# Optimization experiments

Hardware: AMD Instinct MI355X
Metric: run time of the kernel (lower is better)

The kernel has to match this reference:

```python
import jax, jax.numpy as jnp
import numpy as np

BETA = 0.25  # commitment loss weight (standard VQ-VAE beta)


def setup_inputs() -> dict:
    key = jax.random.key(0)
    k1, k2 = jax.random.split(key)
    N, D, Q, K = 131072, 128, 4, 1024
    x = jax.random.normal(k1, (N, D), dtype=jnp.float32)
    codebooks = jax.random.normal(k2, (Q, K, D), dtype=jnp.float32)
    return {"x": x, "codebooks": codebooks}


def reference(x, codebooks):
    """Residual VQ: sequentially quantize the residual against each codebook.

    x:         [N, D] float
    codebooks: [Q, K, D] float (one [K, D] codebook per quantizer stage)
    Returns (x_q [N, D], mean_loss scalar, indices [N, Q] int32).
    """
    sg = jax.lax.stop_gradient

    def stage(carry, E):
        residual, x_q = carry                      # [N, D], [N, D]
        # squared euclidean distances: ||r||^2 - 2 r.E^T + ||E||^2  -> [N, K]
        d = (jnp.sum(residual * residual, axis=1, keepdims=True)
             - 2.0 * (residual @ E.T)
             + jnp.sum(E * E, axis=1))
        idx = jnp.argmin(d, axis=1)                # [N]
        q = E[idx]                                 # [N, D] gather
        # codebook loss + beta * commitment loss
        loss = (jnp.mean((q - sg(residual)) ** 2)
                + BETA * jnp.mean((sg(q) - residual) ** 2))
        # straight-through estimator
        q_st = residual + sg(q - residual)
        return (residual - q_st, x_q + q_st), (loss, idx)

    (_, x_q), (losses, idxs) = jax.lax.scan(
        stage, (x, jnp.zeros_like(x)), codebooks)
    mean_loss = jnp.mean(losses)
    all_indices = jnp.transpose(idxs)              # [Q, N] -> [N, Q], stacked dim=-1
    return x_q, mean_loss, all_indices
```

## Files before the change

kernel.cpp:

```cpp
#include <hip/hip_runtime.h>

#define N_ROWS 131072
#define DIM    128
#define QST    4
#define KC     1024
#define BM     128
#define NTH    256
#define PNTH   256
#define NWAVE  4
#define NCHUNK 64
#define EPS    6e-3f
#define FLAGB  (1 << 16)

typedef _Float16 h8  __attribute__((ext_vector_type(8)));
typedef float    fx4 __attribute__((ext_vector_type(4)));

typedef __attribute__((address_space(3))) void lds_void;
typedef const __attribute__((address_space(1))) void glb_void;

#define MFMA16(a, b, c) __builtin_amdgcn_mfma_f32_16x16x32_f16((a), (b), (c), 0, 0, 0)

__global__ void k_prep(const float* __restrict__ cb,
                       double* __restrict__ cvec64, float* __restrict__ cvec32,
                       _Float16* __restrict__ packB) {
  int gid = blockIdx.x * blockDim.x + threadIdx.x;
  if (gid >= QST * KC) return;
  int q = gid >> 10, code = gid & (KC - 1);
  int ch = code >> 4, n = code & 15;
  const float* e = cb + ((size_t)q * KC + code) * DIM;
  double s = 0.0;
  for (int d = 0; d < DIM; d++) {
    float v = e[d];
    s = fma((double)v, (double)v, s);
    int kt = d >> 5, g = (d >> 3) & 3, j = d & 7;
    int lane = g * 16 + n;
    size_t base = ((size_t)q * NCHUNK + ch) * 4096 + (size_t)kt * 1024 + lane * 8 + j;
    _Float16 hh = (_Float16)v;
    packB[base]       = hh;
    packB[base + 512] = (_Float16)(v - (float)hh);
  }
  cvec64[q * KC + code] = s;
  cvec32[q * KC + code] = (float)s;
}

__global__ __launch_bounds__(NTH, 4) void k_stage(
    int st, const float* rin, float* rout, const float* __restrict__ x,
    const float* __restrict__ cb,
    const double* __restrict__ cvec64, const float* __restrict__ cvec32,
    const _Float16* __restrict__ packB,
    float* __restrict__ oidx, float* __restrict__ lpart, int final_stage)
{
  extern __shared__ float smem[];
  _Float16* Bl      = (_Float16*)smem;
  float*    cvecL   = smem + 6144;
  int*      idxs    = (int*)(smem + 7168);
  double*   redd    = (double*)(smem + 7296);
  int*      redi    = (int*)(smem + 7304);
  float*    redf    = smem + 7308;
  int*      flags   = (int*)(smem + 7312);

  const int tid = threadIdx.x;
  const int lane = tid & 63, wv = tid >> 6;
  const int tx = tid & 15;
  const size_t rowbase = (size_t)blockIdx.x * BM;

  const double*   cq64 = cvec64 + st * KC;
  const float*    cq32 = cvec32 + st * KC;
  const float*    Eq   = cb + (size_t)st * KC * DIM;
  const _Float16* PBq  = packB + (size_t)st * 262144;

  for (int i = tid; i < KC; i += NTH) cvecL[i] = cq32[i];

  h8 ah[2][4], al[2][4];
  #pragma unroll
  for (int rt = 0; rt < 2; rt++) {
    const float* rowp = rin + (rowbase + wv * 32 + rt * 16 + (lane & 15)) * (size_t)DIM
                        + ((lane >> 4) * 8);
    #pragma unroll
    for (int kt = 0; kt < 4; kt++) {
      float4 f0 = *(const float4*)(rowp + kt * 32);
      float4 f1 = *(const float4*)(rowp + kt * 32 + 4);
      float vv[8] = {f0.x, f0.y, f0.z, f0.w, f1.x, f1.y, f1.z, f1.w};
      #pragma unroll
      for (int j = 0; j < 8; j++) {
        _Float16 hh = (_Float16)vv[j];
        ah[rt][kt][j] = hh;
        al[rt][kt][j] = (_Float16)(vv[j] - (float)hh);
      }
    }
  }

  asm volatile("s_waitcnt vmcnt(0) lgkmcnt(0)" ::: "memory");
  __syncthreads();

  auto stageB = [&](int ch, int buf) {
    const _Float16* src = PBq + (size_t)ch * 4096 + wv * 1024 + lane * 8;
    _Float16* dst = Bl + buf * 4096 + wv * 1024;
    #pragma unroll
    for (int i = 0; i < 2; i++)
      __builtin_amdgcn_global_load_lds((glb_void*)(src + i * 512),
                                       (lds_void*)(dst + i * 512), 16, 0, 0);
  };

  float b1[8], b2[8];
  int   i1[8];
  #pragma unroll
  for (int i = 0; i < 8; i++) { b1[i] = 3.4e38f; b2[i] = 3.4e38f; i1[i] = 0; }

  const fx4 zero4 = {0.f, 0.f, 0.f, 0.f};

  stageB(0, 0); stageB(1, 1);

  int buf = 0, bufStage = 2;
  #pragma unroll 1
  for (int ch = 0; ch < NCHUNK; ch++) {
    if (ch < NCHUNK - 1) asm volatile("s_waitcnt vmcnt(2)" ::: "memory");
    else                 asm volatile("s_waitcnt vmcnt(0)" ::: "memory");
    __builtin_amdgcn_s_barrier();
    asm volatile("" ::: "memory");
    if (ch + 2 < NCHUNK) stageB(ch + 2, bufStage);

    const _Float16* Bb = Bl + buf * 4096;
    fx4 acc[2];
    acc[0] = zero4; acc[1] = zero4;

    __builtin_amdgcn_s_setprio(1);
    #pragma unroll
    for (int kt = 0; kt < 4; kt++) {
      const _Float16* p = Bb + (size_t)kt * 1024 + lane * 8;
      h8 bh = *(const h8*)p;
      h8 bl = *(const h8*)(p + 512);
      acc[0] = MFMA16(ah[0][kt], bh, acc[0]);
      acc[1] = MFMA16(ah[1][kt], bh, acc[1]);
      acc[0] = MFMA16(al[0][kt], bh, acc[0]);
      acc[1] = MFMA16(al[1][kt], bh, acc[1]);
      acc[0] = MFMA16(ah[0][kt], bl, acc[0]);
      acc[1] = MFMA16(ah[1][kt], bl, acc[1]);
    }
    __builtin_amdgcn_s_setprio(0);

    {
      int code = ch * 16 + tx;
      float cvv = cvecL[code];
      #pragma unroll
      for (int rt = 0; rt < 2; rt++) {
        #pragma unroll
        for (int j = 0; j < 4; j++) {
          float sc = fmaf(-2.f, acc[rt][j], cvv);
          int r = rt * 4 + j;
          if (sc < b1[r]) { b2[r] = b1[r]; b1[r] = sc; i1[r] = code; }
          else            { b2[r] = fminf(b2[r], sc); }
        }
      }
    }
    buf = (buf == 2) ? 0 : buf + 1;
    bufStage = (bufStage == 2) ? 0 : bufStage + 1;
  }

  #pragma unroll
  for (int m = 1; m < 16; m <<= 1) {
    #pragma unroll
    for (int r = 0; r < 8; r++) {
      float ob1 = __shfl_xor(b1[r], m, 64);
      int   oi1 = __shfl_xor(i1[r], m, 64);
      float ob2 = __shfl_xor(b2[r], m, 64);
      bool take = (ob1 < b1[r]) || (ob1 == b1[r] && oi1 < i1[r]);
      float loser = take ? b1[r] : ob1;
      if (take) { b1[r] = ob1; i1[r] = oi1; }
      b2[r] = fminf(fminf(b2[r], ob2), loser);
    }
  }

  if (tx == 0) {
    int g = lane >> 4;
    #pragma unroll
    for (int rt = 0; rt < 2; rt++)
      #pragma unroll
      for (int j = 0; j < 4; j++) {
        int r = rt * 4 + j;
        int fl = (b2[r] - b1[r] <= EPS) ? FLAGB : 0;
        idxs[wv * 32 + rt * 16 + g * 4 + j] = i1[r] | fl;
      }
  }
  __syncthreads();

  {
    bool pred = (tid < BM) && (idxs[tid] & FLAGB);
    unsigned long long bal = __ballot(pred);
    if (lane == 0) flags[wv] = (bal != 0ull) ? 1 : 0;
  }
  __syncthreads();
  int anyflag = flags[0] | flags[1] | flags[2] | flags[3];
  if (anyflag) {
    for (int row = 0; row < BM; row++) {
      if (!(idxs[row] & FLAGB)) continue;
      const float* rrow = rin + (rowbase + row) * (size_t)DIM;
      double dot[4] = {0.0, 0.0, 0.0, 0.0};
      for (int d = 0; d < DIM; d++) {
        double a = (double)rrow[d];
        #pragma unroll
        for (int c = 0; c < 4; c++)
          dot[c] = fma(a, (double)Eq[(size_t)(tid + c * NTH) * DIM + d], dot[c]);
      }
      double bs = 1e300; int bk = 0;
      #pragma unroll
      for (int c = 0; c < 4; c++) {
        int k = tid + c * NTH;
        double s = fma(-2.0, dot[c], cq64[k]);
        if (s < bs || (s == bs && k < bk)) { bs = s; bk = k; }
      }
      #pragma unroll
      for (int m = 1; m < 64; m <<= 1) {
        double ob = __shfl_xor(bs, m, 64);
        int    ok = __shfl_xor(bk, m, 64);
        if (ob < bs || (ob == bs && ok < bk)) { bs = ob; bk = ok; }
      }
      if (lane == 0) { redd[wv] = bs; redi[wv] = bk; }
      __syncthreads();
      if (tid == 0) {
        double fb = redd[0]; int fk = redi[0];
        #pragma unroll
        for (int w = 1; w < NWAVE; w++) {
          if (redd[w] < fb || (redd[w] == fb && redi[w] < fk)) { fb = redd[w]; fk = redi[w]; }
        }
        idxs[row] = fk;
      }
      __syncthreads();
    }
  }

  {
    float lsum = 0.f;
    #pragma unroll 1
    for (int it = 0; it < 16; it++) {
      int g = it * NTH + tid;
      int row = g >> 5, c4 = g & 31;
      int kidx = idxs[row] & 1023;
      if ((g & 31) == 0) oidx[(rowbase + row) * 4 + st] = (float)kidx;
      float4 ev = *(const float4*)(Eq + (size_t)kidx * DIM + c4 * 4);
      float4 rv = *(const float4*)(rin + (rowbase + row) * (size_t)DIM + c4 * 4);
      float4 dv = make_float4(rv.x - ev.x, rv.y - ev.y, rv.z - ev.z, rv.w - ev.w);
      lsum = fmaf(dv.x, dv.x, lsum);
      lsum = fmaf(dv.y, dv.y, lsum);
      lsum = fmaf(dv.z, dv.z, lsum);
      lsum = fmaf(dv.w, dv.w, lsum);
      float4 wv4 = dv;
      if (final_stage) {
        float4 xv = *(const float4*)(x + (rowbase + row) * (size_t)DIM + c4 * 4);
        wv4 = make_float4(xv.x - dv.x, xv.y - dv.y, xv.z - dv.z, xv.w - dv.w);
      }
      *(float4*)(rout + (rowbase + row) * (size_t)DIM + c4 * 4) = wv4;
    }
    #pragma unroll
    for (int m = 1; m < 64; m <<= 1) lsum += __shfl_xor(lsum, m, 64);
    if (lane == 0) redf[wv] = lsum;
    __syncthreads();
    if (tid == 0) {
      float t = 0.f;
      #pragma unroll
      for (int w = 0; w < NWAVE; w++) t += redf[w];
      lpart[st * (N_ROWS / BM) + blockIdx.x] = t;
    }
  }
}

__global__ void k_loss(const float* __restrict__ part, float* __restrict__ o) {
  __shared__ float red[4];
  int tid = threadIdx.x;
  float s = 0.f;
  for (int i = tid; i < QST * (N_ROWS / BM); i += PNTH) s += part[i];
  #pragma unroll
  for (int m = 1; m < 64; m <<= 1) s += __shfl_xor(s, m, 64);
  if ((tid & 63) == 0) red[tid >> 6] = s;
  __syncthreads();
  if (tid == 0)
    o[0] = (red[0] + red[1] + red[2] + red[3]) *
           (1.25f / ((float)QST * (float)N_ROWS * (float)DIM));
}

extern "C" void kernel_launch(void* const* d_in, const int* in_sizes, int n_in,
                              void* d_out, int out_size, void* d_ws, size_t ws_size,
                              hipStream_t stream) {
  const float* x  = (const float*)d_in[0];
  const float* cb = (const float*)d_in[1];
  float* out = (float*)d_out;
  float* ws  = (float*)d_ws;

  float*    r      = out;
  double*   cvec64 = (double*)ws;
  float*    cvec32 = (float*)(cvec64 + (size_t)QST * KC);
  float*    part   = cvec32 + (size_t)QST * KC;
  _Float16* packB  = (_Float16*)(part + (size_t)QST * (N_ROWS / BM));

  float* out_loss = out + (size_t)N_ROWS * DIM;
  float* out_idx  = out_loss + 1;

  static const size_t SMEM = 7316 * sizeof(float);
  hipFuncSetAttribute(reinterpret_cast<const void*>(k_stage),
                      hipFuncAttributeMaxDynamicSharedMemorySize, (int)SMEM);

  k_prep<<<(QST * KC + PNTH - 1) / PNTH, PNTH, 0, stream>>>(cb, cvec64, cvec32, packB);

  for (int s = 0; s < QST; s++) {
    const float* rin = (s == 0) ? x : r;
    k_stage<<<N_ROWS / BM, NTH, SMEM, stream>>>(s, rin, r, x, cb, cvec64, cvec32,
                                                packB, out_idx, part,
                                                (s == QST - 1) ? 1 : 0);
  }

  k_loss<<<1, PNTH, 0, stream>>>(part, out_loss);
}
```

Measured before the change: 652.3 us.

## Use two waves per block with 64 rows each and per-wave private codebook buffers

The block shrinks from four waves of 32 rows to two waves of 64 rows, so each wave issues four row tiles of MFMAs against every B fragment it reads from LDS, doubling reuse of each fragment. Each wave now stages its own double-buffered copy of the codebook chunk into private LDS and waits only on its own loads, which removes the per-chunk block barrier. The cost is higher register pressure (launch bounds drop to 2 waves per SIMD hint), duplicated global-to-LDS traffic for the codebook per wave, and a longer exact-fallback loop per thread.

```diff
diff --git a/kernel.cpp b/kernel.cpp
--- a/kernel.cpp
+++ b/kernel.cpp
@@ -5,9 +5,8 @@
 #define QST    4
 #define KC     1024
 #define BM     128
-#define NTH    256
+#define NTH    128
 #define PNTH   256
-#define NWAVE  4
 #define NCHUNK 64
 #define EPS    6e-3f
 #define FLAGB  (1 << 16)
@@ -43,7 +42,7 @@
   cvec32[q * KC + code] = (float)s;
 }
 
-__global__ __launch_bounds__(NTH, 4) void k_stage(
+__global__ __launch_bounds__(NTH, 2) void k_stage(
     int st, const float* rin, float* rout, const float* __restrict__ x,
     const float* __restrict__ cb,
     const double* __restrict__ cvec64, const float* __restrict__ cvec32,
@@ -51,17 +50,17 @@
     float* __restrict__ oidx, float* __restrict__ lpart, int final_stage)
 {
   extern __shared__ float smem[];
-  _Float16* Bl      = (_Float16*)smem;
-  float*    cvecL   = smem + 6144;
-  int*      idxs    = (int*)(smem + 7168);
-  double*   redd    = (double*)(smem + 7296);
-  int*      redi    = (int*)(smem + 7304);
-  float*    redf    = smem + 7308;
-  int*      flags   = (int*)(smem + 7312);
+  _Float16* Bl    = (_Float16*)smem;
+  float*    cvecL = smem + 8192;
+  int*      idxs  = (int*)(smem + 9216);
+  double*   redd  = (double*)(smem + 9344);
+  int*      redi  = (int*)(smem + 9348);
+  float*    redf  = smem + 9350;
+  int*      flags = (int*)(smem + 9352);
 
   const int tid = threadIdx.x;
   const int lane = tid & 63, wv = tid >> 6;
-  const int tx = tid & 15;
+  const int tx = lane & 15;
   const size_t rowbase = (size_t)blockIdx.x * BM;
 
   const double*   cq64 = cvec64 + st * KC;
@@ -71,10 +70,10 @@
 
   for (int i = tid; i < KC; i += NTH) cvecL[i] = cq32[i];
 
-  h8 ah[2][4], al[2][4];
+  h8 ah[4][4], al[4][4];
   #pragma unroll
-  for (int rt = 0; rt < 2; rt++) {
-    const float* rowp = rin + (rowbase + wv * 32 + rt * 16 + (lane & 15)) * (size_t)DIM
+  for (int rt = 0; rt < 4; rt++) {
+    const float* rowp = rin + (rowbase + wv * 64 + rt * 16 + (lane & 15)) * (size_t)DIM
                         + ((lane >> 4) * 8);
     #pragma unroll
     for (int kt = 0; kt < 4; kt++) {
@@ -90,39 +89,35 @@
     }
   }
 
-  asm volatile("s_waitcnt vmcnt(0) lgkmcnt(0)" ::: "memory");
   __syncthreads();
 
+  _Float16* myB = Bl + wv * 8192;
   auto stageB = [&](int ch, int buf) {
-    const _Float16* src = PBq + (size_t)ch * 4096 + wv * 1024 + lane * 8;
-    _Float16* dst = Bl + buf * 4096 + wv * 1024;
-    #pragma unroll
-    for (int i = 0; i < 2; i++)
+    const _Float16* src = PBq + (size_t)ch * 4096 + lane * 8;
+    _Float16* dst = myB + buf * 4096;
+    #pragma unroll
+    for (int i = 0; i < 8; i++)
       __builtin_amdgcn_global_load_lds((glb_void*)(src + i * 512),
                                        (lds_void*)(dst + i * 512), 16, 0, 0);
   };
 
-  float b1[8], b2[8];
-  int   i1[8];
+  float b1[16], b2[16];
+  int   i1[16];
   #pragma unroll
-  for (int i = 0; i < 8; i++) { b1[i] = 3.4e38f; b2[i] = 3.4e38f; i1[i] = 0; }
+  for (int i = 0; i < 16; i++) { b1[i] = 3.4e38f; b2[i] = 3.4e38f; i1[i] = 0; }
 
   const fx4 zero4 = {0.f, 0.f, 0.f, 0.f};
 
   stageB(0, 0); stageB(1, 1);
 
-  int buf = 0, bufStage = 2;
   #pragma unroll 1
   for (int ch = 0; ch < NCHUNK; ch++) {
-    if (ch < NCHUNK - 1) asm volatile("s_waitcnt vmcnt(2)" ::: "memory");
+    if (ch < NCHUNK - 1) asm volatile("s_waitcnt vmcnt(8)" ::: "memory");
     else                 asm volatile("s_waitcnt vmcnt(0)" ::: "memory");
-    __builtin_amdgcn_s_barrier();
-    asm volatile("" ::: "memory");
-    if (ch + 2 < NCHUNK) stageB(ch + 2, bufStage);
-
-    const _Float16* Bb = Bl + buf * 4096;
-    fx4 acc[2];
-    acc[0] = zero4; acc[1] = zero4;
+
+    const _Float16* Bb = myB + (ch & 1) * 4096;
+    fx4 acc[4];
+    acc[0] = zero4; acc[1] = zero4; acc[2] = zero4; acc[3] = zero4;
 
     __builtin_amdgcn_s_setprio(1);
     #pragma unroll
@@ -130,20 +125,23 @@
       const _Float16* p = Bb + (size_t)kt * 1024 + lane * 8;
       h8 bh = *(const h8*)p;
       h8 bl = *(const h8*)(p + 512);
-      acc[0] = MFMA16(ah[0][kt], bh, acc[0]);
-      acc[1] = MFMA16(ah[1][kt], bh, acc[1]);
-      acc[0] = MFMA16(al[0][kt], bh, acc[0]);
-      acc[1] = MFMA16(al[1][kt], bh, acc[1]);
-      acc[0] = MFMA16(ah[0][kt], bl, acc[0]);
-      acc[1] = MFMA16(ah[1][kt], bl, acc[1]);
+      #pragma unroll
+      for (int rt = 0; rt < 4; rt++) {
+        acc[rt] = MFMA16(ah[rt][kt], bh, acc[rt]);
+        acc[rt] = MFMA16(al[rt][kt], bh, acc[rt]);
+        acc[rt] = MFMA16(ah[rt][kt], bl, acc[rt]);
+      }
     }
     __builtin_amdgcn_s_setprio(0);
+
+    asm volatile("s_waitcnt lgkmcnt(0)" ::: "memory");
+    if (ch + 2 < NCHUNK) stageB(ch + 2, ch & 1);
 
     {
       int code = ch * 16 + tx;
       float cvv = cvecL[code];
       #pragma unroll
-      for (int rt = 0; rt < 2; rt++) {
+      for (int rt = 0; rt < 4; rt++) {
         #pragma unroll
         for (int j = 0; j < 4; j++) {
           float sc = fmaf(-2.f, acc[rt][j], cvv);
@@ -153,14 +151,12 @@
         }
       }
     }
-    buf = (buf == 2) ? 0 : buf + 1;
-    bufStage = (bufStage == 2) ? 0 : bufStage + 1;
   }
 
   #pragma unroll
   for (int m = 1; m < 16; m <<= 1) {
     #pragma unroll
-    for (int r = 0; r < 8; r++) {
+    for (int r = 0; r < 16; r++) {
       float ob1 = __shfl_xor(b1[r], m, 64);
       int   oi1 = __shfl_xor(i1[r], m, 64);
       float ob2 = __shfl_xor(b2[r], m, 64);
@@ -174,37 +170,37 @@
   if (tx == 0) {
     int g = lane >> 4;
     #pragma unroll
-    for (int rt = 0; rt < 2; rt++)
+    for (int rt = 0; rt < 4; rt++)
       #pragma unroll
       for (int j = 0; j < 4; j++) {
         int r = rt * 4 + j;
         int fl = (b2[r] - b1[r] <= EPS) ? FLAGB : 0;
-        idxs[wv * 32 + rt * 16 + g * 4 + j] = i1[r] | fl;
+        idxs[wv * 64 + rt * 16 + g * 4 + j] = i1[r] | fl;
       }
   }
   __syncthreads();
 
   {
-    bool pred = (tid < BM) && (idxs[tid] & FLAGB);
+    bool pred = (idxs[tid] & FLAGB) != 0;
     unsigned long long bal = __ballot(pred);
     if (lane == 0) flags[wv] = (bal != 0ull) ? 1 : 0;
   }
   __syncthreads();
-  int anyflag = flags[0] | flags[1] | flags[2] | flags[3];
+  int anyflag = flags[0] | flags[1];
   if (anyflag) {
     for (int row = 0; row < BM; row++) {
       if (!(idxs[row] & FLAGB)) continue;
       const float* rrow = rin + (rowbase + row) * (size_t)DIM;
-      double dot[4] = {0.0, 0.0, 0.0, 0.0};
+      double dot[8] = {0.0, 0.0, 0.0, 0.0, 0.0, 0.0, 0.0, 0.0};
       for (int d = 0; d < DIM; d++) {
         double a = (double)rrow[d];
         #pragma unroll
-        for (int c = 0; c < 4; c++)
+        for (int c = 0; c < 8; c++)
           dot[c] = fma(a, (double)Eq[(size_t)(tid + c * NTH) * DIM + d], dot[c]);
       }
       double bs = 1e300; int bk = 0;
       #pragma unroll
-      for (int c = 0; c < 4; c++) {
+      for (int c = 0; c < 8; c++) {
         int k = tid + c * NTH;
         double s = fma(-2.0, dot[c], cq64[k]);
         if (s < bs || (s == bs && k < bk)) { bs = s; bk = k; }
@@ -219,10 +215,7 @@
       __syncthreads();
       if (tid == 0) {
         double fb = redd[0]; int fk = redi[0];
-        #pragma unroll
-        for (int w = 1; w < NWAVE; w++) {
-          if (redd[w] < fb || (redd[w] == fb && redi[w] < fk)) { fb = redd[w]; fk = redi[w]; }
-        }
+        if (redd[1] < fb || (redd[1] == fb && redi[1] < fk)) { fb = redd[1]; fk = redi[1]; }
         idxs[row] = fk;
       }
       __syncthreads();
@@ -232,7 +225,7 @@
   {
     float lsum = 0.f;
     #pragma unroll 1
-    for (int it = 0; it < 16; it++) {
+    for (int it = 0; it < 32; it++) {
       int g = it * NTH + tid;
       int row = g >> 5, c4 = g & 31;
       int kidx = idxs[row] & 1023;
@@ -255,12 +248,7 @@
     for (int m = 1; m < 64; m <<= 1) lsum += __shfl_xor(lsum, m, 64);
     if (lane == 0) redf[wv] = lsum;
     __syncthreads();
-    if (tid == 0) {
-      float t = 0.f;
-      #pragma unroll
-      for (int w = 0; w < NWAVE; w++) t += redf[w];
-      lpart[st * (N_ROWS / BM) + blockIdx.x] = t;
-    }
+    if (tid == 0) lpart[st * (N_ROWS / BM) + blockIdx.x] = redf[0] + redf[1];
   }
 }
 
@@ -295,7 +283,7 @@
   float* out_loss = out + (size_t)N_ROWS * DIM;
   float* out_idx  = out_loss + 1;
 
-  static const size_t SMEM = 7316 * sizeof(float);
+  static const size_t SMEM = 9354 * sizeof(float);
   hipFuncSetAttribute(reinterpret_cast<const void*>(k_stage),
                       hipFuncAttributeMaxDynamicSharedMemorySize, (int)SMEM);
 
```

After: 942.6 us. +44.5%, slower.

## Process codebook chunks in pairs with deeper 8-buffer LDS prefetch ring

Applied to the files above, without the earlier changes.

The main loop now handles two 16-code chunks per iteration, which halves the number of barriers. The LDS staging ring grows from 3 to 8 buffers, with 6 chunks prefetched ahead. Hi and lo-correction MFMA products go into separate accumulators, which cuts the dependency chains and adds ILP. In exchange, LDS use rises to about 70KB and launch bounds drop to 2 blocks per SM, which lowers occupancy.

```diff
diff --git a/kernel.cpp b/kernel.cpp
--- a/kernel.cpp
+++ b/kernel.cpp
@@ -9,6 +9,7 @@
 #define PNTH   256
 #define NWAVE  4
 #define NCHUNK 64
+#define NPAIR  32
 #define EPS    6e-3f
 #define FLAGB  (1 << 16)
 
@@ -43,7 +44,7 @@
   cvec32[q * KC + code] = (float)s;
 }
 
-__global__ __launch_bounds__(NTH, 4) void k_stage(
+__global__ __launch_bounds__(NTH, 2) void k_stage(
     int st, const float* rin, float* rout, const float* __restrict__ x,
     const float* __restrict__ cb,
     const double* __restrict__ cvec64, const float* __restrict__ cvec32,
@@ -51,17 +52,17 @@
     float* __restrict__ oidx, float* __restrict__ lpart, int final_stage)
 {
   extern __shared__ float smem[];
-  _Float16* Bl      = (_Float16*)smem;
-  float*    cvecL   = smem + 6144;
-  int*      idxs    = (int*)(smem + 7168);
-  double*   redd    = (double*)(smem + 7296);
-  int*      redi    = (int*)(smem + 7304);
-  float*    redf    = smem + 7308;
-  int*      flags   = (int*)(smem + 7312);
+  _Float16* Bl    = (_Float16*)smem;
+  float*    cvecL = smem + 16384;
+  int*      idxs  = (int*)(smem + 17408);
+  double*   redd  = (double*)(smem + 17536);
+  int*      redi  = (int*)(smem + 17544);
+  float*    redf  = smem + 17548;
+  int*      flags = (int*)(smem + 17552);
 
   const int tid = threadIdx.x;
   const int lane = tid & 63, wv = tid >> 6;
-  const int tx = tid & 15;
+  const int tx = lane & 15;
   const size_t rowbase = (size_t)blockIdx.x * BM;
 
   const double*   cq64 = cvec64 + st * KC;
@@ -90,12 +91,11 @@
     }
   }
 
-  asm volatile("s_waitcnt vmcnt(0) lgkmcnt(0)" ::: "memory");
   __syncthreads();
 
-  auto stageB = [&](int ch, int buf) {
-    const _Float16* src = PBq + (size_t)ch * 4096 + wv * 1024 + lane * 8;
-    _Float16* dst = Bl + buf * 4096 + wv * 1024;
+  auto stageC = [&](int c) {
+    const _Float16* src = PBq + (size_t)c * 4096 + wv * 1024 + lane * 8;
+    _Float16* dst = Bl + (size_t)(c & 7) * 4096 + wv * 1024;
     #pragma unroll
     for (int i = 0; i < 2; i++)
       __builtin_amdgcn_global_load_lds((glb_void*)(src + i * 512),
@@ -109,52 +109,59 @@
 
   const fx4 zero4 = {0.f, 0.f, 0.f, 0.f};
 
-  stageB(0, 0); stageB(1, 1);
-
-  int buf = 0, bufStage = 2;
+  stageC(0); stageC(1); stageC(2); stageC(3); stageC(4); stageC(5);
+
   #pragma unroll 1
-  for (int ch = 0; ch < NCHUNK; ch++) {
-    if (ch < NCHUNK - 1) asm volatile("s_waitcnt vmcnt(2)" ::: "memory");
-    else                 asm volatile("s_waitcnt vmcnt(0)" ::: "memory");
+  for (int ip = 0; ip < NPAIR; ip++) {
+    if (ip < NPAIR - 2)       asm volatile("s_waitcnt vmcnt(8)" ::: "memory");
+    else if (ip == NPAIR - 2) asm volatile("s_waitcnt vmcnt(4)" ::: "memory");
+    else                      asm volatile("s_waitcnt vmcnt(0)" ::: "memory");
     __builtin_amdgcn_s_barrier();
     asm volatile("" ::: "memory");
-    if (ch + 2 < NCHUNK) stageB(ch + 2, bufStage);
-
-    const _Float16* Bb = Bl + buf * 4096;
-    fx4 acc[2];
-    acc[0] = zero4; acc[1] = zero4;
+    if (ip + 3 < NPAIR) { stageC(2 * (ip + 3)); stageC(2 * (ip + 3) + 1); }
+
+    fx4 acch[2][2], accl[2][2];
+    #pragma unroll
+    for (int g = 0; g < 2; g++)
+      #pragma unroll
+      for (int rt = 0; rt < 2; rt++) { acch[g][rt] = zero4; accl[g][rt] = zero4; }
 
     __builtin_amdgcn_s_setprio(1);
     #pragma unroll
-    for (int kt = 0; kt < 4; kt++) {
-      const _Float16* p = Bb + (size_t)kt * 1024 + lane * 8;
-      h8 bh = *(const h8*)p;
-      h8 bl = *(const h8*)(p + 512);
-      acc[0] = MFMA16(ah[0][kt], bh, acc[0]);
-      acc[1] = MFMA16(ah[1][kt], bh, acc[1]);
-      acc[0] = MFMA16(al[0][kt], bh, acc[0]);
-      acc[1] = MFMA16(al[1][kt], bh, acc[1]);
-      acc[0] = MFMA16(ah[0][kt], bl, acc[0]);
-      acc[1] = MFMA16(ah[1][kt], bl, acc[1]);
+    for (int g = 0; g < 2; g++) {
+      int c = 2 * ip + g;
+      const _Float16* Bb = Bl + (size_t)(c & 7) * 4096;
+      #pragma unroll
+      for (int kt = 0; kt < 4; kt++) {
+        const _Float16* p = Bb + kt * 1024 + lane * 8;
+        h8 bh = *(const h8*)p;
+        h8 bl = *(const h8*)(p + 512);
+        #pragma unroll
+        for (int rt = 0; rt < 2; rt++) {
+          acch[g][rt] = MFMA16(ah[rt][kt], bh, acch[g][rt]);
+          acch[g][rt] = MFMA16(al[rt][kt], bh, acch[g][rt]);
+          accl[g][rt] = MFMA16(ah[rt][kt], bl, accl[g][rt]);
+        }
+      }
     }
     __builtin_amdgcn_s_setprio(0);
 
-    {
-      int code = ch * 16 + tx;
+    #pragma unroll
+    for (int g = 0; g < 2; g++) {
+      int code = (2 * ip + g) * 16 + tx;
       float cvv = cvecL[code];
       #pragma unroll
       for (int rt = 0; rt < 2; rt++) {
         #pragma unroll
         for (int j = 0; j < 4; j++) {
-          float sc = fmaf(-2.f, acc[rt][j], cvv);
+          float s = acch[g][rt][j] + accl[g][rt][j];
+          float sc = fmaf(-2.f, s, cvv);
           int r = rt * 4 + j;
           if (sc < b1[r]) { b2[r] = b1[r]; b1[r] = sc; i1[r] = code; }
           else            { b2[r] = fminf(b2[r], sc); }
         }
       }
     }
-    buf = (buf == 2) ? 0 : buf + 1;
-    bufStage = (bufStage == 2) ? 0 : bufStage + 1;
   }
 
   #pragma unroll
@@ -255,12 +262,8 @@
     for (int m = 1; m < 64; m <<= 1) lsum += __shfl_xor(lsum, m, 64);
     if (lane == 0) redf[wv] = lsum;
     __syncthreads();
-    if (tid == 0) {
-      float t = 0.f;
-      #pragma unroll
-      for (int w = 0; w < NWAVE; w++) t += redf[w];
-      lpart[st * (N_ROWS / BM) + blockIdx.x] = t;
-    }
+    if (tid == 0) lpart[st * (N_ROWS / BM) + blockIdx.x] =
+        redf[0] + redf[1] + redf[2] + redf[3];
   }
 }
 
@@ -295,7 +298,7 @@
   float* out_loss = out + (size_t)N_ROWS * DIM;
   float* out_idx  = out_loss + 1;
 
-  static const size_t SMEM = 7316 * sizeof(float);
+  static const size_t SMEM = 17556 * sizeof(float);
   hipFuncSetAttribute(reinterpret_cast<const void*>(k_stage),
                       hipFuncAttributeMaxDynamicSharedMemorySize, (int)SMEM);
 
```

New measurement: 735.7 us. 1.13x slower.
